# Performance work log

Hardware: AMD Instinct MI355X
Metric: run time of the kernel (lower is better)

## Reference

```python
import jax, jax.numpy as jnp
import numpy as np

HEADS = 4
DIM_HEAD = 32
SCALE = 16.0
EPS = 1e-5  # jax.nn.standardize default


def _standardize(t):
    # standardize over last axis (the flattened x*y*z sequence), per (b, h, d)
    mu = jnp.mean(t, axis=-1, keepdims=True)
    var = jnp.var(t, axis=-1, keepdims=True)
    return (t - mu) * jax.lax.rsqrt(var + EPS)


def setup_inputs() -> dict:
    key = jax.random.key(0)
    k1, k2, k3 = jax.random.split(key, 3)
    dim = 64
    hidden = HEADS * DIM_HEAD  # 128
    b, x, y, z = 2, 16, 16, 16
    inp = jax.random.normal(k1, (b, x, y, z, dim), dtype=jnp.float32)
    # 1x1x1 convs == pointwise channel matmuls; init like flax lecun_normal-ish scale
    w_qkv = jax.random.normal(k2, (dim, 3 * hidden), dtype=jnp.float32) / np.sqrt(dim)
    w_out = jax.random.normal(k3, (hidden, dim), dtype=jnp.float32) / np.sqrt(hidden)
    b_out = jnp.zeros((dim,), dtype=jnp.float32)
    return {"input": inp, "w_qkv": w_qkv, "w_out": w_out, "b_out": b_out}


def reference(input, w_qkv, w_out, b_out):
    b, x, y, z, c = input.shape
    s = x * y * z
    # pointwise conv -> qkv
    qkv = jnp.einsum('bxyzc,cd->bxyzd', input, w_qkv)  # [b,x,y,z,3*hidden]
    q, k, v = jnp.split(qkv, 3, axis=-1)
    # rearrange 'b x y z (h c) -> b h c (x y z)'
    def to_bhds(t):
        return t.reshape(b, s, HEADS, DIM_HEAD).transpose(0, 2, 3, 1)  # [b,h,d,s]
    q, k, v = map(to_bhds, (q, k, v))
    q = _standardize(q)
    k = _standardize(k)
    sim = jnp.einsum('bhdi,bhdj->bhij', q, k) * SCALE  # [b,h,s,s]
    attn = jax.nn.softmax(sim, axis=-1)
    out = jnp.einsum('bhij,bhdj->bhid', attn, v)  # [b,h,s,d]
    # rearrange 'b h (x y z) d -> b x y z (h d)'
    out = out.transpose(0, 2, 1, 3).reshape(b, x, y, z, HEADS * DIM_HEAD)
    return jnp.einsum('bxyzc,co->bxyzo', out, w_out) + b_out
```

## Files before the change

### kernel.cpp

```cpp
#include <hip/hip_runtime.h>
#include <math.h>
#include <stdint.h>


typedef __attribute__((ext_vector_type(8))) short short8;
typedef __attribute__((ext_vector_type(4))) float f32x4;
typedef __attribute__((ext_vector_type(16))) float f32x16;

#define QSCALE 23.083120654223414f

#if __has_builtin(__builtin_amdgcn_exp2f)
#define EXP2F(x) __builtin_amdgcn_exp2f(x)
#else
#define EXP2F(x) exp2f(x)
#endif

__device__ inline uint32_t pack_hilo(float y) {
  uint32_t uy = __float_as_uint(y);
  uint32_t hb = (uy + 0x7fffu + ((uy >> 16) & 1u)) >> 16;
  float hf = __uint_as_float(hb << 16);
  float r = y - hf;
  uint32_t ur = __float_as_uint(r);
  uint32_t lb = (ur + 0x7fffu + ((ur >> 16) & 1u)) >> 16;
  return (hb << 16) | (lb & 0xffffu);
}

__device__ inline ushort f32_to_bf16(float y) {
  uint32_t uy = __float_as_uint(y);
  return (ushort)((uy + 0x7fffu + ((uy >> 16) & 1u)) >> 16);
}

__device__ inline float bpermf(int addr, float v) {
  return __int_as_float(__builtin_amdgcn_ds_bpermute(addr, __float_as_int(v)));
}

__device__ inline short8 as_s8(uint4 v) {
  union { uint4 u; short8 s; } t;
  t.u = v;
  return t.s;
}

__global__ __launch_bounds__(256) void qkv_kernel(const float* __restrict__ in,
                                                  const float* __restrict__ w,
                                                  float* __restrict__ qf,
                                                  float* __restrict__ kf,
                                                  ushort* __restrict__ vfr,
                                                  float* __restrict__ psum,
                                                  float* __restrict__ psq) {
  __shared__ float As[64][68];
  __shared__ float Bs[64][68];
  __shared__ float ssum[64], ssq[64];
  const int ctile = blockIdx.x % 6;
  const int stile = blockIdx.x / 6;
  const int tid = threadIdx.x;
  const int row0 = stile * 64;
  const int sel = ctile >> 1;

  if (tid < 64) { ssum[tid] = 0.f; ssq[tid] = 0.f; }
  for (int idx = tid; idx < 64 * 64; idx += 256) {
    int s = idx >> 6, c = idx & 63;
    As[s][c] = in[(size_t)(row0 + s) * 64 + c];
  }
  for (int idx = tid; idx < 64 * 64; idx += 256) {
    int c = idx >> 6, ch = idx & 63;
    Bs[c][ch] = w[(size_t)c * 384 + ctile * 64 + ch];
  }
  __syncthreads();

  const int ts = tid >> 4, tc = tid & 15;
  float acc[4][4] = {};
  for (int c = 0; c < 64; c += 4) {
    float4 av[4];
#pragma unroll
    for (int a = 0; a < 4; ++a) av[a] = *(const float4*)&As[ts * 4 + a][c];
    const float4 b0 = *(const float4*)&Bs[c + 0][tc * 4];
    const float4 b1 = *(const float4*)&Bs[c + 1][tc * 4];
    const float4 b2 = *(const float4*)&Bs[c + 2][tc * 4];
    const float4 b3 = *(const float4*)&Bs[c + 3][tc * 4];
    const float bm[4][4] = {{b0.x, b0.y, b0.z, b0.w},
                            {b1.x, b1.y, b1.z, b1.w},
                            {b2.x, b2.y, b2.z, b2.w},
                            {b3.x, b3.y, b3.z, b3.w}};
#pragma unroll
    for (int a = 0; a < 4; ++a) {
      const float aw[4] = {av[a].x, av[a].y, av[a].z, av[a].w};
#pragma unroll
      for (int j = 0; j < 4; ++j)
#pragma unroll
        for (int cc = 0; cc < 4; ++cc) acc[a][cc] = fmaf(aw[j], bm[j][cc], acc[a][cc]);
    }
  }

  const int b = row0 >> 12;
  const int sl = (row0 & 4095) + ts * 4;
  const int chg0 = ctile * 64 + tc * 4;

  if (sel < 2) {
    const int hd0 = chg0 & 127;
    const int h = hd0 >> 5, d0 = hd0 & 31;
    float* dst = (sel == 0 ? qf : kf) + ((size_t)(b * 4 + h) * 4096) * 32 + d0;
#pragma unroll
    for (int a = 0; a < 4; ++a) {
      float4 st = make_float4(acc[a][0], acc[a][1], acc[a][2], acc[a][3]);
      *(float4*)&dst[(size_t)(sl + a) * 32] = st;
    }
#pragma unroll
    for (int cc = 0; cc < 4; ++cc) {
      float sm = acc[0][cc] + acc[1][cc] + acc[2][cc] + acc[3][cc];
      float sq = acc[0][cc] * acc[0][cc] + acc[1][cc] * acc[1][cc] +
                 acc[2][cc] * acc[2][cc] + acc[3][cc] * acc[3][cc];
      atomicAdd(&ssum[tc * 4 + cc], sm);
      atomicAdd(&ssq[tc * 4 + cc], sq);
    }
    __syncthreads();
    if (tid < 64) {
      const int ch = (ctile & 1) * 64 + tid;
      const int idx = (((sel * 2 + b) * 128) + ch) * 64 + (stile & 63);
      psum[idx] = ssum[tid];
      psq[idx] = ssq[tid];
    }
  } else {
    __syncthreads();
    float* VT = &As[0][0];
#pragma unroll
    for (int cc = 0; cc < 4; ++cc)
      *(float4*)&VT[(tc * 4 + cc) * 68 + ts * 4] =
          make_float4(acc[0][cc], acc[1][cc], acc[2][cc], acc[3][cc]);
    __syncthreads();
    const int jt0 = (row0 & 4095) >> 5;
#pragma unroll
    for (int hl = 0; hl < 2; ++hl) {
      const int jtl = tid >> 7, c = (tid >> 6) & 1, ln = tid & 63;
      const int d = ln & 31, hh = ln >> 5;
      const int jloc = 32 * jtl + 16 * c + 8 * hh;
      const int ch = hl * 32 + d;
      const float4 f0 = *(const float4*)&VT[ch * 68 + jloc];
      const float4 f1 = *(const float4*)&VT[ch * 68 + jloc + 4];
      uint4 pk;
      pk.x = (uint32_t)f32_to_bf16(f0.x) | ((uint32_t)f32_to_bf16(f0.y) << 16);
      pk.y = (uint32_t)f32_to_bf16(f0.z) | ((uint32_t)f32_to_bf16(f0.w) << 16);
      pk.z = (uint32_t)f32_to_bf16(f1.x) | ((uint32_t)f32_to_bf16(f1.y) << 16);
      pk.w = (uint32_t)f32_to_bf16(f1.z) | ((uint32_t)f32_to_bf16(f1.w) << 16);
      const int h = (ctile - 4) * 2 + hl;
      ushort* dst =
          vfr + (((size_t)((b * 4 + h) * 128 + jt0 + jtl) * 2 + c) * 64 + ln) * 8;
      *(uint4*)dst = pk;
    }
  }
}

__global__ __launch_bounds__(256) void norm_kernel(const float* __restrict__ qf,
                                                   const float* __restrict__ kf,
                                                   ushort* __restrict__ qfr_hi,
                                                   ushort* __restrict__ qfr_lo,
                                                   ushort* __restrict__ kfr_hi,
                                                   ushort* __restrict__ kfr_lo,
                                                   const float* __restrict__ psum,
                                                   const float* __restrict__ psq) {
  const int bx = blockIdx.x;
  const int tensor = bx >> 7;
  const int bh = (bx >> 4) & 7;
  const int s0 = (bx & 15) * 256;
  const int tid = threadIdx.x;
  __shared__ float red[2][32][8];
  __shared__ float tA[32], tB[32];
  {
    const int d = tid >> 3, p = tid & 7;
    const int base = ((tensor * 2 + (bh >> 2)) * 128 + (bh & 3) * 32 + d) * 64 + p * 8;
    float sm = 0.f, sq = 0.f;
#pragma unroll
    for (int e = 0; e < 8; ++e) {
      sm += psum[base + e];
      sq += psq[base + e];
    }
    red[0][d][p] = sm;
    red[1][d][p] = sq;
  }
  __syncthreads();
  if (tid < 32) {
    float sm = 0.f, sq = 0.f;
#pragma unroll
    for (int e = 0; e < 8; ++e) {
      sm += red[0][tid][e];
      sq += red[1][tid][e];
    }
    const float mu = sm * (1.f / 4096.f);
    const float scale = tensor == 0 ? QSCALE : 1.0f;
    const float inv = rsqrtf(sq * (1.f / 4096.f) - mu * mu + 1e-5f) * scale;
    tA[tid] = inv;
    tB[tid] = -mu * inv;
  }
  __syncthreads();

  const float* src = (tensor == 0 ? qf : kf) + (size_t)bh * 4096 * 32;
  ushort* dhi = (tensor == 0 ? qfr_hi : kfr_hi) + (size_t)(bh * 128 + (s0 >> 5)) * 1024;
  ushort* dlo = (tensor == 0 ? qfr_lo : kfr_lo) + (size_t)(bh * 128 + (s0 >> 5)) * 1024;
#pragma unroll
  for (int pass = 0; pass < 4; ++pass) {
    const int idx = tid + pass * 256;
    const int jtl = idx >> 7;
    const int c = (idx >> 6) & 1;
    const int ln = idx & 63;
    const int p = ln & 31, hh = ln >> 5;
    const int row = tensor == 0 ? p : ((p & 0x13) | ((p & 4) << 1) | ((p & 8) >> 1));
    const int s = s0 + 32 * jtl + row;
    const int d0 = 16 * c + 8 * hh;
    const float4 x0 = *(const float4*)&src[(size_t)s * 32 + d0];
    const float4 x1 = *(const float4*)&src[(size_t)s * 32 + d0 + 4];
    const float4 A0 = *(const float4*)&tA[d0];
    const float4 A1 = *(const float4*)&tA[d0 + 4];
    const float4 B0 = *(const float4*)&tB[d0];
    const float4 B1 = *(const float4*)&tB[d0 + 4];
    uint32_t pk[8];
    pk[0] = pack_hilo(fmaf(x0.x, A0.x, B0.x));
    pk[1] = pack_hilo(fmaf(x0.y, A0.y, B0.y));
    pk[2] = pack_hilo(fmaf(x0.z, A0.z, B0.z));
    pk[3] = pack_hilo(fmaf(x0.w, A0.w, B0.w));
    pk[4] = pack_hilo(fmaf(x1.x, A1.x, B1.x));
    pk[5] = pack_hilo(fmaf(x1.y, A1.y, B1.y));
    pk[6] = pack_hilo(fmaf(x1.z, A1.z, B1.z));
    pk[7] = pack_hilo(fmaf(x1.w, A1.w, B1.w));
    uint4 HV, LV;
    HV.x = __builtin_amdgcn_perm(pk[1], pk[0], 0x07060302u);
    HV.y = __builtin_amdgcn_perm(pk[3], pk[2], 0x07060302u);
    HV.z = __builtin_amdgcn_perm(pk[5], pk[4], 0x07060302u);
    HV.w = __builtin_amdgcn_perm(pk[7], pk[6], 0x07060302u);
    LV.x = __builtin_amdgcn_perm(pk[1], pk[0], 0x05040100u);
    LV.y = __builtin_amdgcn_perm(pk[3], pk[2], 0x05040100u);
    LV.z = __builtin_amdgcn_perm(pk[5], pk[4], 0x05040100u);
    LV.w = __builtin_amdgcn_perm(pk[7], pk[6], 0x05040100u);
    const size_t doff = ((size_t)(jtl * 2 + c) * 64 + ln) * 8;
    *(uint4*)(dhi + doff) = HV;
    *(uint4*)(dlo + doff) = LV;
  }
}

__global__ __launch_bounds__(512, 4) void attn_kernel(const ushort* __restrict__ qfr_hi,
                                                      const ushort* __restrict__ qfr_lo,
                                                      const ushort* __restrict__ kfr_hi,
                                                      const ushort* __restrict__ kfr_lo,
                                                      const ushort* __restrict__ vfr,
                                                      float* __restrict__ o) {
  __shared__ float OM[8 * 32 * 36];
  __shared__ float ML[8 * 64];

  const int tid = threadIdx.x;
  const int w = tid >> 6;
  const int js = w & 3;
  const int itl = w >> 2;
  const int lane = tid & 63;
  const int pl = lane & 31, h2 = lane >> 5;
  const int bh = blockIdx.x & 7;
  const int itp = blockIdx.x >> 3;
  const int it = itp * 2 + itl;

  const size_t qbase = (size_t)(bh * 128 + it) * 1024 + lane * 8;
  const short8 qh0 = *(const short8*)(qfr_hi + qbase);
  const short8 qh1 = *(const short8*)(qfr_hi + qbase + 512);
  const short8 ql0 = *(const short8*)(qfr_lo + qbase);
  const short8 ql1 = *(const short8*)(qfr_lo + qbase + 512);

  const int bp32 = (lane ^ 32) << 2;

  const size_t kbase = (size_t)(bh * 128 + js * 32) * 1024 + lane * 8;
  const ushort* kh = kfr_hi + kbase;
  const ushort* kl = kfr_lo + kbase;
  const ushort* vp = vfr + kbase;

  f32x16 oacc;
#pragma unroll
  for (int r = 0; r < 16; ++r) oacc[r] = 0.f;
  float m = -INFINITY, l = 0.f;

  uint4 rk0 = *(const uint4*)(kh);
  uint4 rk1 = *(const uint4*)(kh + 512);
  uint4 rl0 = *(const uint4*)(kl);
  uint4 rl1 = *(const uint4*)(kl + 512);
  uint4 rv0 = *(const uint4*)(vp);
  uint4 rv1 = *(const uint4*)(vp + 512);

  for (int t = 0; t < 32; ++t) {
    const short8 ck0 = as_s8(rk0), ck1 = as_s8(rk1);
    const short8 cl0 = as_s8(rl0), cl1 = as_s8(rl1);
    const short8 cv0 = as_s8(rv0), cv1 = as_s8(rv1);
    {
      const int off = (t + 1) * 1024;
      rk0 = *(const uint4*)(kh + off);
      rk1 = *(const uint4*)(kh + off + 512);
      rl0 = *(const uint4*)(kl + off);
      rl1 = *(const uint4*)(kl + off + 512);
      rv0 = *(const uint4*)(vp + off);
      rv1 = *(const uint4*)(vp + off + 512);
    }

    f32x16 sc;
#pragma unroll
    for (int r = 0; r < 16; ++r) sc[r] = 0.f;
    sc = __builtin_amdgcn_mfma_f32_32x32x16_bf16(ck0, qh0, sc, 0, 0, 0);
    sc = __builtin_amdgcn_mfma_f32_32x32x16_bf16(ck1, qh1, sc, 0, 0, 0);
    sc = __builtin_amdgcn_mfma_f32_32x32x16_bf16(ck0, ql0, sc, 0, 0, 0);
    sc = __builtin_amdgcn_mfma_f32_32x32x16_bf16(ck1, ql1, sc, 0, 0, 0);
    sc = __builtin_amdgcn_mfma_f32_32x32x16_bf16(cl0, qh0, sc, 0, 0, 0);
    sc = __builtin_amdgcn_mfma_f32_32x32x16_bf16(cl1, qh1, sc, 0, 0, 0);

    float mx = sc[0];
#pragma unroll
    for (int r = 1; r < 16; ++r) mx = fmaxf(mx, sc[r]);
    mx = fmaxf(mx, bpermf(bp32, mx));
    const float mn = fmaxf(m, mx);
    const float al = EXP2F(m - mn);
    m = mn;
#pragma unroll
    for (int r = 0; r < 16; ++r) sc[r] = EXP2F(sc[r] - mn);
    float rs = 0.f;
#pragma unroll
    for (int r = 0; r < 16; ++r) rs += sc[r];
    rs += bpermf(bp32, rs);
    l = l * al + rs;
#pragma unroll
    for (int r = 0; r < 16; ++r) oacc[r] *= al;

    uint32_t pk[8];
#pragma unroll
    for (int i = 0; i < 8; ++i)
      pk[i] = __builtin_amdgcn_perm(__float_as_uint(sc[2 * i + 1]),
                                    __float_as_uint(sc[2 * i]), 0x07060302u);
    union { uint32_t u4[4]; short8 s8; } p0, p1;
    p0.u4[0] = pk[0]; p0.u4[1] = pk[1]; p0.u4[2] = pk[2]; p0.u4[3] = pk[3];
    p1.u4[0] = pk[4]; p1.u4[1] = pk[5]; p1.u4[2] = pk[6]; p1.u4[3] = pk[7];

    oacc = __builtin_amdgcn_mfma_f32_32x32x16_bf16(cv0, p0.s8, oacc, 0, 0, 0);
    oacc = __builtin_amdgcn_mfma_f32_32x32x16_bf16(cv1, p1.s8, oacc, 0, 0, 0);
  }

  {
    float* om = OM + (size_t)(w * 32 + pl) * 36;
#pragma unroll
    for (int g = 0; g < 4; ++g)
      *(float4*)&om[4 * h2 + 8 * g] =
          make_float4(oacc[4 * g], oacc[4 * g + 1], oacc[4 * g + 2], oacc[4 * g + 3]);
    if (h2 == 0) {
      ML[w * 64 + pl] = m;
      ML[w * 64 + 32 + pl] = l;
    }
  }
  __syncthreads();
  const int b = bh >> 2, h = bh & 3;
#pragma unroll
  for (int pass = 0; pass < 4; ++pass) {
    const int idx = tid + pass * 512;
    const int itl2 = idx >> 10;
    const int i = (idx >> 5) & 31;
    const int d = idx & 31;
    const int wb = itl2 * 4;
    const float m0 = ML[(wb + 0) * 64 + i], m1 = ML[(wb + 1) * 64 + i];
    const float m2 = ML[(wb + 2) * 64 + i], m3 = ML[(wb + 3) * 64 + i];
    const float l0 = ML[(wb + 0) * 64 + 32 + i], l1 = ML[(wb + 1) * 64 + 32 + i];
    const float l2 = ML[(wb + 2) * 64 + 32 + i], l3 = ML[(wb + 3) * 64 + 32 + i];
    const float M = fmaxf(fmaxf(m0, m1), fmaxf(m2, m3));
    const float w0 = EXP2F(m0 - M), w1 = EXP2F(m1 - M);
    const float w2 = EXP2F(m2 - M), w3 = EXP2F(m3 - M);
    const float L = l0 * w0 + l1 * w1 + l2 * w2 + l3 * w3;
    const float val = (OM[((wb + 0) * 32 + i) * 36 + d] * w0 +
                       OM[((wb + 1) * 32 + i) * 36 + d] * w1 +
                       OM[((wb + 2) * 32 + i) * 36 + d] * w2 +
                       OM[((wb + 3) * 32 + i) * 36 + d] * w3) *
                      (1.001953125f / L);
    const int ig = (itp * 2 + itl2) * 32 + i;
    o[((size_t)(b * 4096) + ig) * 128 + h * 32 + d] = val;
  }
}

__global__ __launch_bounds__(256) void proj_kernel(const float* __restrict__ o,
                                                   const float* __restrict__ w,
                                                   const float* __restrict__ bias,
                                                   float* __restrict__ out) {
  __shared__ float wT[64 * 132];
  const int tid = threadIdx.x;
  for (int idx = tid; idx < 8192; idx += 256) {
    const int c = idx >> 6, col = idx & 63;
    const int g = (c >> 2) ^ ((col >> 3) & 7);
    wT[col * 132 + (g << 2) + (c & 3)] = w[idx];
  }
  __syncthreads();
  const int col = tid & 63;
  const int r = blockIdx.x * 8 + ((tid >> 6) << 1);
  const float* r0 = o + (size_t)r * 128;
  const float* r1 = r0 + 128;
  const int wbase = col * 132;
  const int gx = (col >> 3) & 7;
  float a0 = bias[col], a1 = a0;
  for (int c = 0; c < 128; c += 4) {
    const float4 x0 = *(const float4*)&r0[c];
    const float4 x1 = *(const float4*)&r1[c];
    const float4 wv = *(const float4*)&wT[wbase + ((((c >> 2) ^ gx)) << 2)];
    a0 = fmaf(x0.x, wv.x, a0); a0 = fmaf(x0.y, wv.y, a0);
    a0 = fmaf(x0.z, wv.z, a0); a0 = fmaf(x0.w, wv.w, a0);
    a1 = fmaf(x1.x, wv.x, a1); a1 = fmaf(x1.y, wv.y, a1);
    a1 = fmaf(x1.z, wv.z, a1); a1 = fmaf(x1.w, wv.w, a1);
  }
  out[(size_t)r * 64 + col] = a0;
  out[(size_t)(r + 1) * 64 + col] = a1;
}

extern "C" void kernel_launch(void* const* d_in, const int* in_sizes, int n_in,
                              void* d_out, int out_size, void* d_ws, size_t ws_size,
                              hipStream_t stream) {
  const float* input = (const float*)d_in[0];
  const float* w_qkv = (const float*)d_in[1];
  const float* w_out = (const float*)d_in[2];
  const float* b_out = (const float*)d_in[3];

  char* W = (char*)d_ws;
  float* qf = (float*)(W + 0);
  float* kf = (float*)(W + (4u << 20));
  ushort* kfr_hi = (ushort*)(W + (8u << 20));
  ushort* kfr_lo = (ushort*)(W + (10u << 20));
  ushort* vfr = (ushort*)(W + (12u << 20));
  ushort* qfr_hi = (ushort*)(W + (14u << 20));
  ushort* qfr_lo = (ushort*)(W + (16u << 20));
  float* psum = (float*)(W + (18u << 20));
  float* psq = (float*)(W + (18u << 20) + (128u << 10));
  float* ob = qf;
  float* out = (float*)d_out;

  hipLaunchKernelGGL(qkv_kernel, dim3(768), dim3(256), 0, stream, input, w_qkv, qf, kf,
                     vfr, psum, psq);
  hipLaunchKernelGGL(norm_kernel, dim3(256), dim3(256), 0, stream, qf, kf, qfr_hi,
                     qfr_lo, kfr_hi, kfr_lo, psum, psq);
  hipLaunchKernelGGL(attn_kernel, dim3(512), dim3(512), 0, stream, qfr_hi, qfr_lo,
                     kfr_hi, kfr_lo, vfr, ob);
  hipLaunchKernelGGL(proj_kernel, dim3(1024), dim3(256), 0, stream, ob, w_out, b_out, out);
}
```

Measured before the change: 140.6 us.

## Fuse Q normalization into attention and split keys across eight waves

The norm kernel now only reorders and normalizes K. For Q it just computes per-channel scale and shift, and the attention kernel loads raw fp32 Q and builds the hi/lo bf16 fragments in registers. Each attention block now handles one 32-row query tile, and its eight waves each take one eighth of the keys (16 tiles), which doubles the grid and adds an eight-way merge at the end. Max and sum reductions become tree-shaped. This removes the Q hi/lo round trip through global memory and halves the serial key loop, at the cost of more blocks that each reload K/V and a larger merge step.

```diff
diff --git a/kernel.cpp b/kernel.cpp
--- a/kernel.cpp
+++ b/kernel.cpp
@@ -149,24 +149,36 @@
   }
 }
 
-__global__ __launch_bounds__(256) void norm_kernel(const float* __restrict__ qf,
-                                                   const float* __restrict__ kf,
-                                                   ushort* __restrict__ qfr_hi,
-                                                   ushort* __restrict__ qfr_lo,
+__global__ __launch_bounds__(256) void norm_kernel(const float* __restrict__ kf,
                                                    ushort* __restrict__ kfr_hi,
                                                    ushort* __restrict__ kfr_lo,
                                                    const float* __restrict__ psum,
-                                                   const float* __restrict__ psq) {
+                                                   const float* __restrict__ psq,
+                                                   float* __restrict__ qA,
+                                                   float* __restrict__ qB) {
   const int bx = blockIdx.x;
-  const int tensor = bx >> 7;
-  const int bh = (bx >> 4) & 7;
-  const int s0 = (bx & 15) * 256;
   const int tid = threadIdx.x;
+  if (bx == 128) {
+    const int base = (((tid >> 7) * 128) + (tid & 127)) * 64;
+    float sm = 0.f, sq = 0.f;
+#pragma unroll 8
+    for (int e = 0; e < 64; ++e) {
+      sm += psum[base + e];
+      sq += psq[base + e];
+    }
+    const float mu = sm * (1.f / 4096.f);
+    const float inv = rsqrtf(sq * (1.f / 4096.f) - mu * mu + 1e-5f) * QSCALE;
+    qA[tid] = inv;
+    qB[tid] = -mu * inv;
+    return;
+  }
   __shared__ float red[2][32][8];
   __shared__ float tA[32], tB[32];
+  const int bh = bx >> 4;
+  const int s0 = (bx & 15) * 256;
   {
     const int d = tid >> 3, p = tid & 7;
-    const int base = ((tensor * 2 + (bh >> 2)) * 128 + (bh & 3) * 32 + d) * 64 + p * 8;
+    const int base = ((2 + (bh >> 2)) * 128 + (bh & 3) * 32 + d) * 64 + p * 8;
     float sm = 0.f, sq = 0.f;
 #pragma unroll
     for (int e = 0; e < 8; ++e) {
@@ -185,16 +197,15 @@
       sq += red[1][tid][e];
     }
     const float mu = sm * (1.f / 4096.f);
-    const float scale = tensor == 0 ? QSCALE : 1.0f;
-    const float inv = rsqrtf(sq * (1.f / 4096.f) - mu * mu + 1e-5f) * scale;
+    const float inv = rsqrtf(sq * (1.f / 4096.f) - mu * mu + 1e-5f);
     tA[tid] = inv;
     tB[tid] = -mu * inv;
   }
   __syncthreads();
 
-  const float* src = (tensor == 0 ? qf : kf) + (size_t)bh * 4096 * 32;
-  ushort* dhi = (tensor == 0 ? qfr_hi : kfr_hi) + (size_t)(bh * 128 + (s0 >> 5)) * 1024;
-  ushort* dlo = (tensor == 0 ? qfr_lo : kfr_lo) + (size_t)(bh * 128 + (s0 >> 5)) * 1024;
+  const float* src = kf + (size_t)bh * 4096 * 32;
+  ushort* dhi = kfr_hi + (size_t)(bh * 128 + (s0 >> 5)) * 1024;
+  ushort* dlo = kfr_lo + (size_t)(bh * 128 + (s0 >> 5)) * 1024;
 #pragma unroll
   for (int pass = 0; pass < 4; ++pass) {
     const int idx = tid + pass * 256;
@@ -202,7 +213,7 @@
     const int c = (idx >> 6) & 1;
     const int ln = idx & 63;
     const int p = ln & 31, hh = ln >> 5;
-    const int row = tensor == 0 ? p : ((p & 0x13) | ((p & 4) << 1) | ((p & 8) >> 1));
+    const int row = (p & 0x13) | ((p & 4) << 1) | ((p & 8) >> 1);
     const int s = s0 + 32 * jtl + row;
     const int d0 = 16 * c + 8 * hh;
     const float4 x0 = *(const float4*)&src[(size_t)s * 32 + d0];
@@ -235,8 +246,9 @@
   }
 }
 
-__global__ __launch_bounds__(512, 4) void attn_kernel(const ushort* __restrict__ qfr_hi,
-                                                      const ushort* __restrict__ qfr_lo,
+__global__ __launch_bounds__(512, 4) void attn_kernel(const float* __restrict__ qf,
+                                                      const float* __restrict__ qA,
+                                                      const float* __restrict__ qB,
                                                       const ushort* __restrict__ kfr_hi,
                                                       const ushort* __restrict__ kfr_lo,
                                                       const ushort* __restrict__ vfr,
@@ -246,23 +258,48 @@
 
   const int tid = threadIdx.x;
   const int w = tid >> 6;
-  const int js = w & 3;
-  const int itl = w >> 2;
   const int lane = tid & 63;
   const int pl = lane & 31, h2 = lane >> 5;
   const int bh = blockIdx.x & 7;
-  const int itp = blockIdx.x >> 3;
-  const int it = itp * 2 + itl;
-
-  const size_t qbase = (size_t)(bh * 128 + it) * 1024 + lane * 8;
-  const short8 qh0 = *(const short8*)(qfr_hi + qbase);
-  const short8 qh1 = *(const short8*)(qfr_hi + qbase + 512);
-  const short8 ql0 = *(const short8*)(qfr_lo + qbase);
-  const short8 ql1 = *(const short8*)(qfr_lo + qbase + 512);
+  const int it = blockIdx.x >> 3;
+
+  const int irow = it * 32 + pl;
+  const float* qptr = qf + ((size_t)bh * 4096 + irow) * 32;
+  short8 qh0, ql0, qh1, ql1;
+  {
+    const int da = 8 * h2, db = 16 + 8 * h2;
+    const float4 x0 = *(const float4*)(qptr + da);
+    const float4 x1 = *(const float4*)(qptr + da + 4);
+    const float4 x2 = *(const float4*)(qptr + db);
+    const float4 x3 = *(const float4*)(qptr + db + 4);
+    const float4 A0 = *(const float4*)&qA[bh * 32 + da];
+    const float4 A1 = *(const float4*)&qA[bh * 32 + da + 4];
+    const float4 A2 = *(const float4*)&qA[bh * 32 + db];
+    const float4 A3 = *(const float4*)&qA[bh * 32 + db + 4];
+    const float4 B0 = *(const float4*)&qB[bh * 32 + da];
+    const float4 B1 = *(const float4*)&qB[bh * 32 + da + 4];
+    const float4 B2 = *(const float4*)&qB[bh * 32 + db];
+    const float4 B3 = *(const float4*)&qB[bh * 32 + db + 4];
+    const float y0[8] = {fmaf(x0.x, A0.x, B0.x), fmaf(x0.y, A0.y, B0.y),
+                         fmaf(x0.z, A0.z, B0.z), fmaf(x0.w, A0.w, B0.w),
+                         fmaf(x1.x, A1.x, B1.x), fmaf(x1.y, A1.y, B1.y),
+                         fmaf(x1.z, A1.z, B1.z), fmaf(x1.w, A1.w, B1.w)};
+    const float y1[8] = {fmaf(x2.x, A2.x, B2.x), fmaf(x2.y, A2.y, B2.y),
+                         fmaf(x2.z, A2.z, B2.z), fmaf(x2.w, A2.w, B2.w),
+                         fmaf(x3.x, A3.x, B3.x), fmaf(x3.y, A3.y, B3.y),
+                         fmaf(x3.z, A3.z, B3.z), fmaf(x3.w, A3.w, B3.w)};
+#pragma unroll
+    for (int j = 0; j < 8; ++j) {
+      uint32_t p0 = pack_hilo(y0[j]);
+      uint32_t p1 = pack_hilo(y1[j]);
+      qh0[j] = (short)(p0 >> 16); ql0[j] = (short)(p0 & 0xffff);
+      qh1[j] = (short)(p1 >> 16); ql1[j] = (short)(p1 & 0xffff);
+    }
+  }
 
   const int bp32 = (lane ^ 32) << 2;
 
-  const size_t kbase = (size_t)(bh * 128 + js * 32) * 1024 + lane * 8;
+  const size_t kbase = (size_t)(bh * 128 + w * 16) * 1024 + lane * 8;
   const ushort* kh = kfr_hi + kbase;
   const ushort* kl = kfr_lo + kbase;
   const ushort* vp = vfr + kbase;
@@ -279,7 +316,7 @@
   uint4 rv0 = *(const uint4*)(vp);
   uint4 rv1 = *(const uint4*)(vp + 512);
 
-  for (int t = 0; t < 32; ++t) {
+  for (int t = 0; t < 16; ++t) {
     const short8 ck0 = as_s8(rk0), ck1 = as_s8(rk1);
     const short8 cl0 = as_s8(rl0), cl1 = as_s8(rl1);
     const short8 cv0 = as_s8(rv0), cv1 = as_s8(rv1);
@@ -303,18 +340,24 @@
     sc = __builtin_amdgcn_mfma_f32_32x32x16_bf16(cl0, qh0, sc, 0, 0, 0);
     sc = __builtin_amdgcn_mfma_f32_32x32x16_bf16(cl1, qh1, sc, 0, 0, 0);
 
-    float mx = sc[0];
-#pragma unroll
-    for (int r = 1; r < 16; ++r) mx = fmaxf(mx, sc[r]);
+    float t8[8];
+#pragma unroll
+    for (int r = 0; r < 8; ++r) t8[r] = fmaxf(sc[r], sc[r + 8]);
+#pragma unroll
+    for (int r = 0; r < 4; ++r) t8[r] = fmaxf(t8[r], t8[r + 4]);
+    float mx = fmaxf(fmaxf(t8[0], t8[1]), fmaxf(t8[2], t8[3]));
     mx = fmaxf(mx, bpermf(bp32, mx));
     const float mn = fmaxf(m, mx);
     const float al = EXP2F(m - mn);
     m = mn;
 #pragma unroll
     for (int r = 0; r < 16; ++r) sc[r] = EXP2F(sc[r] - mn);
-    float rs = 0.f;
-#pragma unroll
-    for (int r = 0; r < 16; ++r) rs += sc[r];
+    float s8v[8];
+#pragma unroll
+    for (int r = 0; r < 8; ++r) s8v[r] = sc[r] + sc[r + 8];
+#pragma unroll
+    for (int r = 0; r < 4; ++r) s8v[r] = s8v[r] + s8v[r + 4];
+    float rs = (s8v[0] + s8v[1]) + (s8v[2] + s8v[3]);
     rs += bpermf(bp32, rs);
     l = l * al + rs;
 #pragma unroll
@@ -347,26 +390,25 @@
   __syncthreads();
   const int b = bh >> 2, h = bh & 3;
 #pragma unroll
-  for (int pass = 0; pass < 4; ++pass) {
+  for (int pass = 0; pass < 2; ++pass) {
     const int idx = tid + pass * 512;
-    const int itl2 = idx >> 10;
-    const int i = (idx >> 5) & 31;
+    const int i = idx >> 5;
     const int d = idx & 31;
-    const int wb = itl2 * 4;
-    const float m0 = ML[(wb + 0) * 64 + i], m1 = ML[(wb + 1) * 64 + i];
-    const float m2 = ML[(wb + 2) * 64 + i], m3 = ML[(wb + 3) * 64 + i];
-    const float l0 = ML[(wb + 0) * 64 + 32 + i], l1 = ML[(wb + 1) * 64 + 32 + i];
-    const float l2 = ML[(wb + 2) * 64 + 32 + i], l3 = ML[(wb + 3) * 64 + 32 + i];
-    const float M = fmaxf(fmaxf(m0, m1), fmaxf(m2, m3));
-    const float w0 = EXP2F(m0 - M), w1 = EXP2F(m1 - M);
-    const float w2 = EXP2F(m2 - M), w3 = EXP2F(m3 - M);
-    const float L = l0 * w0 + l1 * w1 + l2 * w2 + l3 * w3;
-    const float val = (OM[((wb + 0) * 32 + i) * 36 + d] * w0 +
-                       OM[((wb + 1) * 32 + i) * 36 + d] * w1 +
-                       OM[((wb + 2) * 32 + i) * 36 + d] * w2 +
-                       OM[((wb + 3) * 32 + i) * 36 + d] * w3) *
-                      (1.001953125f / L);
-    const int ig = (itp * 2 + itl2) * 32 + i;
+    float mk[8];
+#pragma unroll
+    for (int k = 0; k < 8; ++k) mk[k] = ML[k * 64 + i];
+    float M = mk[0];
+#pragma unroll
+    for (int k = 1; k < 8; ++k) M = fmaxf(M, mk[k]);
+    float L = 0.f, acc = 0.f;
+#pragma unroll
+    for (int k = 0; k < 8; ++k) {
+      const float wk = EXP2F(mk[k] - M);
+      L += ML[k * 64 + 32 + i] * wk;
+      acc += OM[(k * 32 + i) * 36 + d] * wk;
+    }
+    const float val = acc * (1.001953125f / L);
+    const int ig = it * 32 + i;
     o[((size_t)(b * 4096) + ig) * 128 + h * 32 + d] = val;
   }
 }
@@ -417,18 +459,18 @@
   ushort* kfr_hi = (ushort*)(W + (8u << 20));
   ushort* kfr_lo = (ushort*)(W + (10u << 20));
   ushort* vfr = (ushort*)(W + (12u << 20));
-  ushort* qfr_hi = (ushort*)(W + (14u << 20));
-  ushort* qfr_lo = (ushort*)(W + (16u << 20));
-  float* psum = (float*)(W + (18u << 20));
-  float* psq = (float*)(W + (18u << 20) + (128u << 10));
-  float* ob = qf;
+  float* psum = (float*)(W + (14u << 20));
+  float* psq = (float*)(W + (14u << 20) + (128u << 10));
+  float* qA = (float*)(W + (14u << 20) + (256u << 10));
+  float* qB = qA + 256;
+  float* ob = kf;
   float* out = (float*)d_out;
 
   hipLaunchKernelGGL(qkv_kernel, dim3(768), dim3(256), 0, stream, input, w_qkv, qf, kf,
                      vfr, psum, psq);
-  hipLaunchKernelGGL(norm_kernel, dim3(256), dim3(256), 0, stream, qf, kf, qfr_hi,
-                     qfr_lo, kfr_hi, kfr_lo, psum, psq);
-  hipLaunchKernelGGL(attn_kernel, dim3(512), dim3(512), 0, stream, qfr_hi, qfr_lo,
+  hipLaunchKernelGGL(norm_kernel, dim3(129), dim3(256), 0, stream, kf, kfr_hi, kfr_lo,
+                     psum, psq, qA, qB);
+  hipLaunchKernelGGL(attn_kernel, dim3(1024), dim3(512), 0, stream, qf, qA, qB,
                      kfr_hi, kfr_lo, vfr, ob);
   hipLaunchKernelGGL(proj_kernel, dim3(1024), dim3(256), 0, stream, ob, w_out, b_out, out);
 }
```

Measured after the change: 150.0 us. 6.7% more time.
